# Kernel optimization log

Hardware: AMD Instinct MI355X
Metric: run time of the kernel (lower is better)

## Reference

```python
import jax, jax.numpy as jnp
import numpy as np

NB_HEAD = 16
SIZE_PER_HEAD = 64
D_MODEL = NB_HEAD * SIZE_PER_HEAD  # 1024
B, L = 2, 2048
NEG_BIG = 1e12


def setup_inputs() -> dict:
    key = jax.random.key(0)
    ks = jax.random.split(key, 8)
    return {
        "Q_seq": jax.random.normal(ks[0], (B, L, D_MODEL), dtype=jnp.float32),
        "K_seq": jax.random.normal(ks[1], (B, L, D_MODEL), dtype=jnp.float32),
        "V_seq": jax.random.normal(ks[2], (B, L, D_MODEL), dtype=jnp.float32),
        "q_len": jax.random.randint(ks[3], (B, 1), 1, L, dtype=jnp.int32),
        "v_len": jax.random.randint(ks[4], (B, 1), 1, L, dtype=jnp.int32),
        "WQ": jax.random.normal(ks[5], (D_MODEL, D_MODEL), dtype=jnp.float32) * 0.02,
        "WK": jax.random.normal(ks[6], (D_MODEL, D_MODEL), dtype=jnp.float32) * 0.02,
        "WV": jax.random.normal(ks[7], (D_MODEL, D_MODEL), dtype=jnp.float32) * 0.02,
    }


def _len_mask(lens, length, dtype):
    # Keras code: mask = 1 - cumsum(one_hot(len, L)) -> 1 for pos < len, 0 otherwise
    return (jnp.arange(length)[None, :] < lens).astype(dtype)  # [B, L]


def reference(Q_seq, K_seq, V_seq, q_len, v_len, WQ, WK, WV):
    Bq, Lq, _ = Q_seq.shape
    Lk = K_seq.shape[1]
    # QKV projections, split heads: [B, H, L, D]
    q = (Q_seq @ WQ).reshape(Bq, Lq, NB_HEAD, SIZE_PER_HEAD).transpose(0, 2, 1, 3)
    k = (K_seq @ WK).reshape(Bq, Lk, NB_HEAD, SIZE_PER_HEAD).transpose(0, 2, 1, 3)
    v = (V_seq @ WV).reshape(Bq, Lk, NB_HEAD, SIZE_PER_HEAD).transpose(0, 2, 1, 3)
    # scaled dot-product scores [B, H, Lq, Lk]
    scores = jnp.einsum("bhqd,bhkd->bhqk", q, k) / np.float32(SIZE_PER_HEAD ** 0.5)
    # additive key-length mask (V_len), matching Mask(..., 'add')
    kmask = _len_mask(v_len, Lk, scores.dtype)  # [B, Lk]
    scores = scores - (1.0 - kmask)[:, None, None, :] * np.float32(NEG_BIG)
    A = jax.nn.softmax(scores, axis=-1)
    # attention output, merge heads: [B, Lq, H*D]
    O = jnp.einsum("bhqk,bhkd->bqhd", A, v).reshape(Bq, Lq, D_MODEL)
    # multiplicative query-length mask (Q_len), matching Mask(..., 'mul')
    qmask = _len_mask(q_len, Lq, O.dtype)  # [B, Lq]
    return O * qmask[:, :, None]
```

## Files before the change

kernel.cpp:

```cpp
#include <hip/hip_runtime.h>
#include <cstddef>

#define NB_HEAD 16
#define HEAD_DIM 64
#define D_MODEL 1024
#define BATCH 2
#define SEQ 2048
#define MROWS (BATCH * SEQ)
#define NSPLIT 3

typedef __bf16 bf16x8 __attribute__((ext_vector_type(8)));
typedef __bf16 bf16x4 __attribute__((ext_vector_type(4)));
typedef __bf16 bf16x2 __attribute__((ext_vector_type(2)));
typedef float  f32x4  __attribute__((ext_vector_type(4)));

#define XEL ((size_t)MROWS * D_MODEL)
#define WEL ((size_t)D_MODEL * D_MODEL)

#define QSCALE 0.18033688011112042f

static __device__ __forceinline__ size_t xchunk(int row, int k) {
    return ((size_t)(row >> 4) * 32 + (k >> 5)) * 512 + ((k >> 3) & 3) * 128 + (row & 15) * 8 + (k & 7);
}
static __device__ __forceinline__ size_t qkbase(int bh, int row16, int dc) {
    return ((size_t)(bh * 128 + row16) * 2 + dc) * 512;
}
static __device__ __forceinline__ size_t qkelem(int bh, int row, int d) {
    return qkbase(bh, row >> 4, d >> 5) + ((d >> 3) & 3) * 128 + (row & 15) * 8 + (d & 7);
}
static __device__ __forceinline__ size_t vbase(int bh, int d16, int kc) {
    return ((size_t)(bh * 4 + d16) * 64 + kc) * 512;
}
static __device__ __forceinline__ size_t velem(int bh, int d, int key) {
    return vbase(bh, d >> 4, key >> 5) + ((key >> 3) & 3) * 128 + (d & 15) * 8 + (key & 7);
}

static __device__ __forceinline__ void split_bf16(float x, __bf16& h, __bf16& l) {
    h = (__bf16)x;
    l = (__bf16)(x - (float)h);
}

static __device__ __forceinline__ void gload_lds16(const __bf16* g, __bf16* l) {
    __builtin_amdgcn_global_load_lds((const __attribute__((address_space(1))) void*)g,
                                     (__attribute__((address_space(3))) void*)l,
                                     16, 0, 0);
}

__global__ __launch_bounds__(256) void conv_wt_kernel(
    const float* __restrict__ W0, const float* __restrict__ W1,
    const float* __restrict__ W2,
    __bf16* __restrict__ hi, __bf16* __restrict__ lo)
{
    __shared__ float tile[64][65];
    const int t  = threadIdx.x;
    const int k0 = blockIdx.x * 64;
    const int n0 = blockIdx.y * 64;
    const int z  = blockIdx.z;
    const float* W = (z == 0) ? W0 : ((z == 1) ? W1 : W2);
    __bf16* hz = hi + (size_t)z * WEL;
    __bf16* lz = lo + (size_t)z * WEL;

    #pragma unroll
    for (int p = 0; p < 4; ++p) {
        const int e = (p * 256 + t) * 4;
        const int r = e >> 6, c = e & 63;
        const float4 v = *(const float4*)(W + (size_t)(k0 + r) * D_MODEL + n0 + c);
        tile[r][c] = v.x; tile[r][c + 1] = v.y; tile[r][c + 2] = v.z; tile[r][c + 3] = v.w;
    }
    __syncthreads();
    #pragma unroll
    for (int p = 0; p < 4; ++p) {
        const int e = (p * 256 + t) * 4;
        const int n = e >> 6, kc = e & 63;
        __bf16 h[4], l[4];
        #pragma unroll
        for (int u = 0; u < 4; ++u) split_bf16(tile[kc + u][n], h[u], l[u]);
        const size_t a = xchunk(n0 + n, k0 + kc);
        *(bf16x4*)(hz + a) = (bf16x4){h[0], h[1], h[2], h[3]};
        *(bf16x4*)(lz + a) = (bf16x4){l[0], l[1], l[2], l[3]};
    }
}

__global__ __launch_bounds__(256) void conv_x_kernel(
    const float* __restrict__ X0, const float* __restrict__ X1,
    const float* __restrict__ X2,
    const int* __restrict__ q_len, const int* __restrict__ v_len,
    __bf16* __restrict__ xhi, __bf16* __restrict__ xlo)
{
    const int z = blockIdx.y;
    const size_t e = ((size_t)blockIdx.x * 256 + threadIdx.x) * 8;
    const int l = (int)(e >> 10), k = (int)(e & 1023);
    const int bb = l >> 11, lb = l & (SEQ - 1);
    const int len = (z == 0) ? q_len[bb] : v_len[bb];
    if (lb >= ((len + 127) & ~127)) return;

    const float* X = (z == 0) ? X0 : ((z == 1) ? X1 : X2);
    const float4 v0 = *(const float4*)(X + e);
    const float4 v1 = *(const float4*)(X + e + 4);
    const float xs[8] = {v0.x, v0.y, v0.z, v0.w, v1.x, v1.y, v1.z, v1.w};
    bf16x8 h8, l8;
    #pragma unroll
    for (int u = 0; u < 8; ++u) { __bf16 h_, l_; split_bf16(xs[u], h_, l_); h8[u] = h_; l8[u] = l_; }
    const size_t a = z * XEL + xchunk(l, k);
    *(bf16x8*)(xhi + a) = h8;
    *(bf16x8*)(xlo + a) = l8;
}

__global__ __launch_bounds__(256, 3) void proj_mfma_kernel(
    const __bf16* __restrict__ Xhi, const __bf16* __restrict__ Xlo,
    const __bf16* __restrict__ Wchi, const __bf16* __restrict__ Wclo,
    const int* __restrict__ q_len, const int* __restrict__ v_len,
    __bf16* __restrict__ qch, __bf16* __restrict__ qcl,
    __bf16* __restrict__ kch, __bf16* __restrict__ kcl,
    __bf16* __restrict__ vch, __bf16* __restrict__ vcl)
{
    __shared__ __align__(16) __bf16 lds[2][24][512];

    const int t    = threadIdx.x;
    const int wave = t >> 6, lane = t & 63;
    const int li   = lane & 15, grp = lane >> 4;
    const int wm   = wave >> 1, wn = wave & 1;
    const int m0   = blockIdx.x * 128;
    const int n0   = blockIdx.y * 64;
    const int z    = blockIdx.z;
    const int bb   = m0 >> 11;
    const int l0   = m0 & (SEQ - 1);
    const int need = (z == 0) ? q_len[bb] : v_len[bb];
    if (l0 >= need) return;

    const __bf16* Xh = Xhi + z * XEL;
    const __bf16* Xl = Xlo + z * XEL;
    const __bf16* Wh = Wchi + z * WEL;
    const __bf16* Wl = Wclo + z * WEL;

    const __bf16* gs[6];
    #pragma unroll
    for (int u = 0; u < 6; ++u) {
        const int c = u * 4 + wave;
        const __bf16* src;
        int idx;
        if (c < 8)       { src = Xh; idx = (m0 >> 4) + c; }
        else if (c < 16) { src = Xl; idx = (m0 >> 4) + (c - 8); }
        else if (c < 20) { src = Wh; idx = (n0 >> 4) + (c - 16); }
        else             { src = Wl; idx = (n0 >> 4) + (c - 20); }
        gs[u] = src + (size_t)idx * 32 * 512 + (size_t)lane * 8;
    }

    auto STAGE = [&](int buf, int kc) {
        #pragma unroll
        for (int u = 0; u < 6; ++u)
            gload_lds16(gs[u] + (size_t)kc * 512, &lds[buf][u * 4 + wave][0]);
    };

    f32x4 acc[4][2] = {};

    STAGE(0, 0);
    __syncthreads();

    #pragma unroll 2
    for (int kc = 0; kc < 32; ++kc) {
        const int cur = kc & 1;
        if (kc < 31) STAGE(cur ^ 1, kc + 1);

        bf16x8 ah[4], al4[4], bh2[2], bl2[2];
        #pragma unroll
        for (int i = 0; i < 4; ++i) {
            ah[i]  = *(const bf16x8*)&lds[cur][(wm << 2) + i][lane * 8];
            al4[i] = *(const bf16x8*)&lds[cur][8 + (wm << 2) + i][lane * 8];
        }
        #pragma unroll
        for (int j = 0; j < 2; ++j) {
            bh2[j] = *(const bf16x8*)&lds[cur][16 + (wn << 1) + j][lane * 8];
            bl2[j] = *(const bf16x8*)&lds[cur][20 + (wn << 1) + j][lane * 8];
        }
        #pragma unroll
        for (int j = 0; j < 2; ++j) {
            #pragma unroll
            for (int i = 0; i < 4; ++i) {
                acc[i][j] = __builtin_amdgcn_mfma_f32_16x16x32_bf16(ah[i],  bh2[j], acc[i][j], 0, 0, 0);
                acc[i][j] = __builtin_amdgcn_mfma_f32_16x16x32_bf16(ah[i],  bl2[j], acc[i][j], 0, 0, 0);
                acc[i][j] = __builtin_amdgcn_mfma_f32_16x16x32_bf16(al4[i], bh2[j], acc[i][j], 0, 0, 0);
            }
        }
        __syncthreads();
    }

    #pragma unroll
    for (int j = 0; j < 2; ++j) {
        const int cg = n0 + wn * 32 + j * 16 + li;
        const int hd = cg >> 6, d = cg & 63;
        const int bhI = bb * NB_HEAD + hd;
        #pragma unroll
        for (int i = 0; i < 4; ++i) {
            #pragma unroll
            for (int r = 0; r < 4; ++r) {
                const int rg = m0 + wm * 64 + i * 16 + grp * 4 + r;
                const int lg = rg & (SEQ - 1);
                __bf16 h_, l_;
                if (z == 0) {
                    split_bf16(acc[i][j][r] * QSCALE, h_, l_);
                    const size_t a = qkelem(bhI, lg, d);
                    qch[a] = h_; qcl[a] = l_;
                } else if (z == 1) {
                    split_bf16(acc[i][j][r], h_, l_);
                    const size_t a = qkelem(bhI, lg, d);
                    kch[a] = h_; kcl[a] = l_;
                } else {
                    split_bf16(acc[i][j][r], h_, l_);
                    const size_t a = velem(bhI, d, lg);
                    vch[a] = h_; vcl[a] = l_;
                }
            }
        }
    }
}

__global__ __launch_bounds__(256, 2) void attn_mfma_kernel(
    const __bf16* __restrict__ qch, const __bf16* __restrict__ qcl,
    const __bf16* __restrict__ kch, const __bf16* __restrict__ kcl,
    const __bf16* __restrict__ vch, const __bf16* __restrict__ vcl,
    const int* __restrict__ q_len, const int* __restrict__ v_len,
    float* __restrict__ Opart, float* __restrict__ Mbuf, float* __restrict__ Lbuf)
{
    __shared__ __align__(16) __bf16 Ps[128][72];

    const int t = threadIdx.x;
    const int wq = t >> 6, lane = t & 63;
    const int grp = lane >> 4, li = lane & 15;
    const int hh = blockIdx.x;
    const int split = (int)(blockIdx.y % NSPLIT);
    const int q0 = (int)(blockIdx.y / NSPLIT) * 128;
    const int b  = blockIdx.z;
    const int qlen = q_len[b], vlen = v_len[b];
    const int bh = b * NB_HEAD + hh;
    const int qbase = q0 + wq * 32;

    if (qbase >= qlen) return;

    bf16x8 onesv;
    #pragma unroll
    for (int u = 0; u < 8; ++u) onesv[u] = (__bf16)1.0f;

    bf16x8 qh[2][2], ql[2][2];
    #pragma unroll
    for (int s = 0; s < 2; ++s)
        #pragma unroll
        for (int ks = 0; ks < 2; ++ks) {
            const size_t a = qkbase(bh, (qbase >> 4) + s, ks) + lane * 8;
            qh[s][ks] = *(const bf16x8*)(qch + a);
            ql[s][ks] = *(const bf16x8*)(qcl + a);
        }

    f32x4 O[2][4] = {};
    float m_s[2] = {-1e30f, -1e30f};
    float l_s[2][4];
    #pragma unroll
    for (int s = 0; s < 2; ++s)
        #pragma unroll
        for (int r = 0; r < 4; ++r) l_s[s][r] = 0.f;

    const int nktT = (vlen + 63) >> 6;
    const int part = (nktT + NSPLIT - 1) / NSPLIT;
    const int tBeg = split * part;
    const int tEnd = (nktT < tBeg + part) ? nktT : (tBeg + part);

    for (int tt = tBeg; tt < tEnd; ++tt) {
        const int k0 = tt * 64;
        const bool full = (k0 + 64 <= vlen);

        f32x4 sacc[2][4] = {};
        #pragma unroll
        for (int ks = 0; ks < 2; ++ks) {
            bf16x8 kh_[4], kl_[4];
            #pragma unroll
            for (int j = 0; j < 4; ++j) {
                const size_t a = qkbase(bh, (k0 >> 4) + j, ks) + lane * 8;
                kh_[j] = *(const bf16x8*)(kch + a);
                kl_[j] = *(const bf16x8*)(kcl + a);
            }
            __builtin_amdgcn_s_setprio(1);
            #pragma unroll
            for (int j = 0; j < 4; ++j)
                #pragma unroll
                for (int s = 0; s < 2; ++s) {
                    sacc[s][j] = __builtin_amdgcn_mfma_f32_16x16x32_bf16(kh_[j], qh[s][ks], sacc[s][j], 0, 0, 0);
                    sacc[s][j] = __builtin_amdgcn_mfma_f32_16x16x32_bf16(kl_[j], qh[s][ks], sacc[s][j], 0, 0, 0);
                    sacc[s][j] = __builtin_amdgcn_mfma_f32_16x16x32_bf16(kh_[j], ql[s][ks], sacc[s][j], 0, 0, 0);
                }
            __builtin_amdgcn_s_setprio(0);
        }

        bf16x8 vh_[2][4], vl_[2][4];
        #pragma unroll
        for (int ks = 0; ks < 2; ++ks)
            #pragma unroll
            for (int j = 0; j < 4; ++j) {
                const size_t a = vbase(bh, j, (k0 >> 5) + ks) + lane * 8;
                vh_[ks][j] = *(const bf16x8*)(vch + a);
                vl_[ks][j] = *(const bf16x8*)(vcl + a);
            }

        float mx[2];
        int defer = 1;
        #pragma unroll
        for (int s = 0; s < 2; ++s) {
            if (!full) {
                #pragma unroll
                for (int j = 0; j < 4; ++j) {
                    const int keyb = k0 + j * 16 + grp * 4;
                    #pragma unroll
                    for (int r = 0; r < 4; ++r)
                        if (keyb + r >= vlen) sacc[s][j][r] = -1e30f;
                }
            }
            float m0_ = -1e30f;
            #pragma unroll
            for (int j = 0; j < 4; ++j)
                #pragma unroll
                for (int r = 0; r < 4; ++r) m0_ = fmaxf(m0_, sacc[s][j][r]);
            m0_ = fmaxf(m0_, __shfl_xor(m0_, 16));
            m0_ = fmaxf(m0_, __shfl_xor(m0_, 32));
            mx[s] = m0_;
            defer &= (m0_ - m_s[s] <= 8.f) ? 1 : 0;
        }

        if (!__all(defer)) {
            #pragma unroll
            for (int s = 0; s < 2; ++s) {
                const float mn = fmaxf(m_s[s], mx[s]);
                const float alq = exp2f(m_s[s] - mn);
                m_s[s] = mn;
                #pragma unroll
                for (int r = 0; r < 4; ++r) {
                    const float alr = __shfl(alq, grp * 4 + r);
                    l_s[s][r] *= alr;
                    #pragma unroll
                    for (int j = 0; j < 4; ++j) O[s][j][r] *= alr;
                }
            }
        }

        #pragma unroll
        for (int s = 0; s < 2; ++s) {
            const int row = wq * 32 + s * 16 + li;
            #pragma unroll
            for (int j = 0; j < 4; ++j) {
                const int col = j * 16 + grp * 4;
                bf16x2 w01, w23;
                w01[0] = (__bf16)exp2f(sacc[s][j][0] - m_s[s]);
                w01[1] = (__bf16)exp2f(sacc[s][j][1] - m_s[s]);
                w23[0] = (__bf16)exp2f(sacc[s][j][2] - m_s[s]);
                w23[1] = (__bf16)exp2f(sacc[s][j][3] - m_s[s]);
                *(bf16x2*)&Ps[row][col]     = w01;
                *(bf16x2*)&Ps[row][col + 2] = w23;
            }
        }
        asm volatile("s_waitcnt lgkmcnt(0)" ::: "memory");

        bf16x8 pa[2][2];
        #pragma unroll
        for (int s = 0; s < 2; ++s)
            #pragma unroll
            for (int ks = 0; ks < 2; ++ks)
                pa[s][ks] = *(const bf16x8*)&Ps[wq * 32 + s * 16 + li][ks * 32 + grp * 8];

        __builtin_amdgcn_s_setprio(1);
        #pragma unroll
        for (int s = 0; s < 2; ++s) {
            f32x4 lsum = {};
            lsum = __builtin_amdgcn_mfma_f32_16x16x32_bf16(pa[s][0], onesv, lsum, 0, 0, 0);
            lsum = __builtin_amdgcn_mfma_f32_16x16x32_bf16(pa[s][1], onesv, lsum, 0, 0, 0);
            #pragma unroll
            for (int r = 0; r < 4; ++r) l_s[s][r] += lsum[r];
        }

        #pragma unroll
        for (int ks = 0; ks < 2; ++ks)
            #pragma unroll
            for (int j = 0; j < 4; ++j)
                #pragma unroll
                for (int s = 0; s < 2; ++s) {
                    O[s][j] = __builtin_amdgcn_mfma_f32_16x16x32_bf16(pa[s][ks], vh_[ks][j], O[s][j], 0, 0, 0);
                    O[s][j] = __builtin_amdgcn_mfma_f32_16x16x32_bf16(pa[s][ks], vl_[ks][j], O[s][j], 0, 0, 0);
                }
        __builtin_amdgcn_s_setprio(0);
    }

    const size_t osplit = (size_t)split * MROWS * D_MODEL;
    #pragma unroll
    for (int s = 0; s < 2; ++s)
        #pragma unroll
        for (int r = 0; r < 4; ++r) {
            const int q = qbase + s * 16 + grp * 4 + r;
            if (q < qlen) {
                #pragma unroll
                for (int j = 0; j < 4; ++j)
                    Opart[osplit + ((size_t)b * SEQ + q) * D_MODEL + hh * HEAD_DIM + j * 16 + li] = O[s][j][r];
                if (li == 0) {
                    const size_t mi = (((size_t)split * BATCH + b) * NB_HEAD + hh) * SEQ + q;
                    Lbuf[mi] = l_s[s][r];
                }
            }
        }
    #pragma unroll
    for (int s = 0; s < 2; ++s) {
        const int q = qbase + s * 16 + li;
        if (grp == 0 && q < qlen) {
            const size_t mi = (((size_t)split * BATCH + b) * NB_HEAD + hh) * SEQ + q;
            Mbuf[mi] = m_s[s];
        }
    }
}

__global__ __launch_bounds__(256) void attn_merge_kernel(
    const float* __restrict__ Opart, const float* __restrict__ Mbuf,
    const float* __restrict__ Lbuf, const int* __restrict__ q_len,
    float* __restrict__ out)
{
    const int row = blockIdx.x;
    const int b = row >> 11, q = row & (SEQ - 1);
    const int col = threadIdx.x * 4;
    const int hh = col >> 6;
    const size_t oidx = (size_t)row * D_MODEL + col;

    float4 o = make_float4(0.f, 0.f, 0.f, 0.f);
    if (q < q_len[b]) {
        const size_t mlsz = (size_t)BATCH * NB_HEAD * SEQ;
        const size_t mi = ((size_t)b * NB_HEAD + hh) * SEQ + q;
        float ms[NSPLIT], ls[NSPLIT];
        float M = -1e30f;
        #pragma unroll
        for (int s = 0; s < NSPLIT; ++s) {
            ms[s] = Mbuf[s * mlsz + mi];
            ls[s] = Lbuf[s * mlsz + mi];
            M = fmaxf(M, ms[s]);
        }
        float denom = 0.f;
        float w[NSPLIT];
        #pragma unroll
        for (int s = 0; s < NSPLIT; ++s) {
            w[s] = exp2f(ms[s] - M);
            denom += ls[s] * w[s];
        }
        const float inv = 1.f / denom;
        float acc[4] = {0.f, 0.f, 0.f, 0.f};
        #pragma unroll
        for (int s = 0; s < NSPLIT; ++s) {
            const float4 a = *(const float4*)(Opart + (size_t)s * MROWS * D_MODEL + oidx);
            acc[0] += a.x * w[s]; acc[1] += a.y * w[s];
            acc[2] += a.z * w[s]; acc[3] += a.w * w[s];
        }
        o.x = acc[0] * inv; o.y = acc[1] * inv; o.z = acc[2] * inv; o.w = acc[3] * inv;
    }
    *(float4*)(out + oidx) = o;
}

extern "C" void kernel_launch(void* const* d_in, const int* in_sizes, int n_in,
                              void* d_out, int out_size, void* d_ws, size_t ws_size,
                              hipStream_t stream)
{
    (void)in_sizes; (void)n_in; (void)out_size; (void)ws_size;
    const float* Q_seq = (const float*)d_in[0];
    const float* K_seq = (const float*)d_in[1];
    const float* V_seq = (const float*)d_in[2];
    const int*   q_len = (const int*)d_in[3];
    const int*   v_len = (const int*)d_in[4];
    const float* WQ    = (const float*)d_in[5];
    const float* WK    = (const float*)d_in[6];
    const float* WV    = (const float*)d_in[7];
    float* out = (float*)d_out;

    __bf16* wchi = (__bf16*)d_ws;
    __bf16* wclo = wchi + 3 * WEL;
    __bf16* xhi_ = wclo + 3 * WEL;
    __bf16* xlo_ = xhi_ + 3 * XEL;
    __bf16* qch_ = xlo_ + 3 * XEL;
    __bf16* qcl_ = qch_ + XEL;
    __bf16* kch_ = qcl_ + XEL;
    __bf16* kcl_ = kch_ + XEL;
    __bf16* vch_ = kcl_ + XEL;
    __bf16* vcl_ = vch_ + XEL;

    float* Opart = (float*)xhi_;
    float* Mbuf  = (float*)wchi;
    float* Lbuf  = Mbuf + (size_t)NSPLIT * BATCH * NB_HEAD * SEQ;

    dim3 blk(256);

    dim3 cg(D_MODEL / 64, D_MODEL / 64, 3);
    conv_wt_kernel<<<cg, blk, 0, stream>>>(WQ, WK, WV, wchi, wclo);

    dim3 xg((unsigned)(XEL / 2048), 3);
    conv_x_kernel<<<xg, blk, 0, stream>>>(Q_seq, K_seq, V_seq, q_len, v_len, xhi_, xlo_);

    dim3 pg(MROWS / 128, D_MODEL / 64, 3);
    proj_mfma_kernel<<<pg, blk, 0, stream>>>(xhi_, xlo_, wchi, wclo, q_len, v_len,
                                             qch_, qcl_, kch_, kcl_, vch_, vcl_);

    dim3 ag(NB_HEAD, (SEQ / 128) * NSPLIT, BATCH);
    attn_mfma_kernel<<<ag, blk, 0, stream>>>(qch_, qcl_, kch_, kcl_, vch_, vcl_,
                                             q_len, v_len, Opart, Mbuf, Lbuf);

    attn_merge_kernel<<<dim3(MROWS), blk, 0, stream>>>(Opart, Mbuf, Lbuf, q_len, out);
}
```

Before: 260.1 us.

## Triple-buffer projection GEMM and load weight fragments directly into registers

The projection GEMM switches from a double-buffered LDS pipeline to a fully unrolled three-stage pipeline that prefetches two k-chunks ahead. It uses explicit vmcnt waits and a single barrier per step instead of syncthreads. Weight (B) fragments are no longer staged through LDS; each wave loads its own hi/lo weight chunks straight into registers, which shrinks LDS to 16 rows per stage. The intent is to hide global-load latency and cut LDS traffic, at the cost of more VGPRs for the three register sets of B fragments, which could hurt occupancy at 3 blocks/CU, and more redundant global reads of W across waves.

Result: no change. 263.3 us (+1.2%).

```diff
diff --git a/kernel.cpp b/kernel.cpp
--- a/kernel.cpp
+++ b/kernel.cpp
@@ -114,7 +114,7 @@
     __bf16* __restrict__ kch, __bf16* __restrict__ kcl,
     __bf16* __restrict__ vch, __bf16* __restrict__ vcl)
 {
-    __shared__ __align__(16) __bf16 lds[2][24][512];
+    __shared__ __align__(16) __bf16 lds[3][16][512];
 
     const int t    = threadIdx.x;
     const int wave = t >> 6, lane = t & 63;
@@ -133,57 +133,103 @@
     const __bf16* Wh = Wchi + z * WEL;
     const __bf16* Wl = Wclo + z * WEL;
 
-    const __bf16* gs[6];
-    #pragma unroll
-    for (int u = 0; u < 6; ++u) {
-        const int c = u * 4 + wave;
-        const __bf16* src;
-        int idx;
-        if (c < 8)       { src = Xh; idx = (m0 >> 4) + c; }
-        else if (c < 16) { src = Xl; idx = (m0 >> 4) + (c - 8); }
-        else if (c < 20) { src = Wh; idx = (n0 >> 4) + (c - 16); }
-        else             { src = Wl; idx = (n0 >> 4) + (c - 20); }
-        gs[u] = src + (size_t)idx * 32 * 512 + (size_t)lane * 8;
-    }
-
-    auto STAGE = [&](int buf, int kc) {
-        #pragma unroll
-        for (int u = 0; u < 6; ++u)
-            gload_lds16(gs[u] + (size_t)kc * 512, &lds[buf][u * 4 + wave][0]);
-    };
+    const __bf16* gsA0;
+    const __bf16* gsA1;
+    const __bf16* gsA2;
+    const __bf16* gsA3;
+    {
+        const __bf16* tmp[4];
+        #pragma unroll
+        for (int u = 0; u < 4; ++u) {
+            const int c = u * 4 + wave;
+            const __bf16* src = (c < 8) ? Xh : Xl;
+            const int idx = (m0 >> 4) + (c & 7);
+            tmp[u] = src + (size_t)idx * 32 * 512 + (size_t)lane * 8;
+        }
+        gsA0 = tmp[0]; gsA1 = tmp[1]; gsA2 = tmp[2]; gsA3 = tmp[3];
+    }
+
+    const __bf16* gBh0 = Wh + (size_t)((n0 >> 4) + wn * 2 + 0) * 32 * 512 + (size_t)lane * 8;
+    const __bf16* gBh1 = Wh + (size_t)((n0 >> 4) + wn * 2 + 1) * 32 * 512 + (size_t)lane * 8;
+    const __bf16* gBl0 = Wl + (size_t)((n0 >> 4) + wn * 2 + 0) * 32 * 512 + (size_t)lane * 8;
+    const __bf16* gBl1 = Wl + (size_t)((n0 >> 4) + wn * 2 + 1) * 32 * 512 + (size_t)lane * 8;
+
+    bf16x8 b0ha, b0hb, b0la, b0lb;
+    bf16x8 b1ha, b1hb, b1la, b1lb;
+    bf16x8 b2ha, b2hb, b2la, b2lb;
 
     f32x4 acc[4][2] = {};
 
-    STAGE(0, 0);
-    __syncthreads();
-
-    #pragma unroll 2
-    for (int kc = 0; kc < 32; ++kc) {
-        const int cur = kc & 1;
-        if (kc < 31) STAGE(cur ^ 1, kc + 1);
-
-        bf16x8 ah[4], al4[4], bh2[2], bl2[2];
-        #pragma unroll
-        for (int i = 0; i < 4; ++i) {
-            ah[i]  = *(const bf16x8*)&lds[cur][(wm << 2) + i][lane * 8];
-            al4[i] = *(const bf16x8*)&lds[cur][8 + (wm << 2) + i][lane * 8];
-        }
-        #pragma unroll
-        for (int j = 0; j < 2; ++j) {
-            bh2[j] = *(const bf16x8*)&lds[cur][16 + (wn << 1) + j][lane * 8];
-            bl2[j] = *(const bf16x8*)&lds[cur][20 + (wn << 1) + j][lane * 8];
-        }
-        #pragma unroll
-        for (int j = 0; j < 2; ++j) {
-            #pragma unroll
-            for (int i = 0; i < 4; ++i) {
-                acc[i][j] = __builtin_amdgcn_mfma_f32_16x16x32_bf16(ah[i],  bh2[j], acc[i][j], 0, 0, 0);
-                acc[i][j] = __builtin_amdgcn_mfma_f32_16x16x32_bf16(ah[i],  bl2[j], acc[i][j], 0, 0, 0);
-                acc[i][j] = __builtin_amdgcn_mfma_f32_16x16x32_bf16(al4[i], bh2[j], acc[i][j], 0, 0, 0);
-            }
-        }
-        __syncthreads();
-    }
+#define STAGE_A(BUF, KC) do { \
+    gload_lds16(gsA0 + (size_t)(KC) * 512, &lds[BUF][ 0 + wave][0]); \
+    gload_lds16(gsA1 + (size_t)(KC) * 512, &lds[BUF][ 4 + wave][0]); \
+    gload_lds16(gsA2 + (size_t)(KC) * 512, &lds[BUF][ 8 + wave][0]); \
+    gload_lds16(gsA3 + (size_t)(KC) * 512, &lds[BUF][12 + wave][0]); \
+} while (0)
+
+#define LOADB(S, KC) do { \
+    b##S##ha = *(const bf16x8*)(gBh0 + (size_t)(KC) * 512); \
+    b##S##hb = *(const bf16x8*)(gBh1 + (size_t)(KC) * 512); \
+    b##S##la = *(const bf16x8*)(gBl0 + (size_t)(KC) * 512); \
+    b##S##lb = *(const bf16x8*)(gBl1 + (size_t)(KC) * 512); \
+} while (0)
+
+#define COMPUTE(BUF, S) do { \
+    bf16x8 a_h[4], a_l[4]; \
+    _Pragma("unroll") \
+    for (int i_ = 0; i_ < 4; ++i_) { \
+        a_h[i_] = *(const bf16x8*)&lds[BUF][(wm << 2) + i_][lane * 8]; \
+        a_l[i_] = *(const bf16x8*)&lds[BUF][8 + (wm << 2) + i_][lane * 8]; \
+    } \
+    _Pragma("unroll") \
+    for (int i_ = 0; i_ < 4; ++i_) { \
+        acc[i_][0] = __builtin_amdgcn_mfma_f32_16x16x32_bf16(a_h[i_], b##S##ha, acc[i_][0], 0, 0, 0); \
+        acc[i_][0] = __builtin_amdgcn_mfma_f32_16x16x32_bf16(a_h[i_], b##S##la, acc[i_][0], 0, 0, 0); \
+        acc[i_][0] = __builtin_amdgcn_mfma_f32_16x16x32_bf16(a_l[i_], b##S##ha, acc[i_][0], 0, 0, 0); \
+        acc[i_][1] = __builtin_amdgcn_mfma_f32_16x16x32_bf16(a_h[i_], b##S##hb, acc[i_][1], 0, 0, 0); \
+        acc[i_][1] = __builtin_amdgcn_mfma_f32_16x16x32_bf16(a_h[i_], b##S##lb, acc[i_][1], 0, 0, 0); \
+        acc[i_][1] = __builtin_amdgcn_mfma_f32_16x16x32_bf16(a_l[i_], b##S##hb, acc[i_][1], 0, 0, 0); \
+    } \
+} while (0)
+
+#define STEP_PF(KC, CUR, PF) do { \
+    STAGE_A(PF, (KC) + 2); \
+    LOADB(PF, (KC) + 2); \
+    __builtin_amdgcn_sched_barrier(0); \
+    COMPUTE(CUR, CUR); \
+    asm volatile("s_waitcnt vmcnt(8)" ::: "memory"); \
+    __builtin_amdgcn_s_barrier(); \
+    __builtin_amdgcn_sched_barrier(0); \
+} while (0)
+
+    STAGE_A(0, 0); LOADB(0, 0);
+    STAGE_A(1, 1); LOADB(1, 1);
+    asm volatile("s_waitcnt vmcnt(8)" ::: "memory");
+    __builtin_amdgcn_s_barrier();
+    __builtin_amdgcn_sched_barrier(0);
+
+    STEP_PF( 0, 0, 2); STEP_PF( 1, 1, 0); STEP_PF( 2, 2, 1);
+    STEP_PF( 3, 0, 2); STEP_PF( 4, 1, 0); STEP_PF( 5, 2, 1);
+    STEP_PF( 6, 0, 2); STEP_PF( 7, 1, 0); STEP_PF( 8, 2, 1);
+    STEP_PF( 9, 0, 2); STEP_PF(10, 1, 0); STEP_PF(11, 2, 1);
+    STEP_PF(12, 0, 2); STEP_PF(13, 1, 0); STEP_PF(14, 2, 1);
+    STEP_PF(15, 0, 2); STEP_PF(16, 1, 0); STEP_PF(17, 2, 1);
+    STEP_PF(18, 0, 2); STEP_PF(19, 1, 0); STEP_PF(20, 2, 1);
+    STEP_PF(21, 0, 2); STEP_PF(22, 1, 0); STEP_PF(23, 2, 1);
+    STEP_PF(24, 0, 2); STEP_PF(25, 1, 0); STEP_PF(26, 2, 1);
+    STEP_PF(27, 0, 2); STEP_PF(28, 1, 0); STEP_PF(29, 2, 1);
+
+    COMPUTE(0, 0);
+    asm volatile("s_waitcnt vmcnt(0)" ::: "memory");
+    __builtin_amdgcn_s_barrier();
+    __builtin_amdgcn_sched_barrier(0);
+
+    COMPUTE(1, 1);
+
+#undef STEP_PF
+#undef COMPUTE
+#undef LOADB
+#undef STAGE_A
 
     #pragma unroll
     for (int j = 0; j < 2; ++j) {
```
